# Optimization experiments

Measured on AMD Instinct MI355X. Metric: run time of the kernel, lower is better.

## Reference

```python
import jax, jax.numpy as jnp
import numpy as np

IN_FEATURES = 4096
OUT_FEATURES = 8192
LUT_SIZE = 65536  # 256 * 256 two-level codebook


def setup_inputs() -> dict:
    key = jax.random.key(0)
    k_x, k_b, k_f, k_s, k_l = jax.random.split(key, 5)
    x = jax.random.normal(k_x, (2, 256, IN_FEATURES), dtype=jnp.float32)
    base_idx = jax.random.randint(k_b, (OUT_FEATURES, IN_FEATURES), 0, 256, dtype=jnp.int32)
    fine_idx = jax.random.randint(k_f, (OUT_FEATURES, IN_FEATURES), 0, 256, dtype=jnp.int32)
    scale = jax.random.uniform(k_s, (OUT_FEATURES, 1), dtype=jnp.float32)
    lut = jax.random.normal(k_l, (LUT_SIZE,), dtype=jnp.float32)
    return {"x": x, "base_idx": base_idx, "fine_idx": fine_idx, "scale": scale, "lut": lut}


def reference(x, base_idx, fine_idx, scale, lut):
    # Two-level LUT dequant: combined 16-bit index = base*256 + fine
    combined_idx = base_idx * 256 + fine_idx              # [out, in] int32
    weights = lut[combined_idx] * scale                   # [out, in] fp32, per-row scale
    # F.linear(x, weights) == x @ weights.T
    return jnp.einsum('bsi,oi->bso', x, weights)
```

## Files before the change

kernel.cpp:

```cpp
#include <hip/hip_runtime.h>

typedef unsigned short ushort_t;
typedef unsigned int   uint32;
typedef __attribute__((ext_vector_type(8)))  short short8;
typedef __attribute__((ext_vector_type(4)))  float floatx4;
typedef __attribute__((ext_vector_type(16))) float floatx16;

#define IN_F   4096
#define OUT_F  8192
#define M_TOT  512

__device__ __forceinline__ ushort_t f2bf(float f) {
    uint32 u = __builtin_bit_cast(uint32, f);
    u += 0x7FFFu + ((u >> 16) & 1u);
    return (ushort_t)(u >> 16);
}
__device__ __forceinline__ uint32 pack2bf(float a, float b) {
    return (uint32)f2bf(a) | ((uint32)f2bf(b) << 16);
}

__global__ void cvt_x_kernel(const float* __restrict__ x, ushort_t* __restrict__ xb) {
    int i = (blockIdx.x * 256 + threadIdx.x) * 8;
    float4 v0 = *(const float4*)(x + i);
    float4 v1 = *(const float4*)(x + i + 4);
    short8 s;
    s[0] = (short)f2bf(v0.x); s[1] = (short)f2bf(v0.y);
    s[2] = (short)f2bf(v0.z); s[3] = (short)f2bf(v0.w);
    s[4] = (short)f2bf(v1.x); s[5] = (short)f2bf(v1.y);
    s[6] = (short)f2bf(v1.z); s[7] = (short)f2bf(v1.w);
    *(short8*)(xb + i) = s;
}

__global__ __launch_bounds__(1024, 4)
void dequant_kernel(const int* __restrict__ base_idx, const int* __restrict__ fine_idx,
                    const float* __restrict__ lut, ushort_t* __restrict__ wq)
{
    __shared__ ushort_t sh_lut[65536];
    const int tid = threadIdx.x;
#pragma unroll
    for (int i = tid * 4; i < 65536; i += 1024 * 4) {
        float4 v = *(const float4*)(lut + i);
        *(uint32*)&sh_lut[i]     = pack2bf(v.x, v.y);
        *(uint32*)&sh_lut[i + 2] = pack2bf(v.z, v.w);
    }

    const int row = blockIdx.x * 32 + (tid >> 5);
    const int c0  = (tid & 31) * 8;
    const int* bp = base_idx + (size_t)row * IN_F + c0;
    const int* fp = fine_idx + (size_t)row * IN_F + c0;
    ushort_t*  op = wq       + (size_t)row * IN_F + c0;

    int4 cb[4][2], cf[4][2];
#pragma unroll
    for (int d = 0; d < 4; ++d) {
        cb[d][0] = *(const int4*)(bp + d * 256);
        cb[d][1] = *(const int4*)(bp + d * 256 + 4);
        cf[d][0] = *(const int4*)(fp + d * 256);
        cf[d][1] = *(const int4*)(fp + d * 256 + 4);
    }
    __syncthreads();

#pragma unroll
    for (int u = 0; u < 16; ++u) {
        const int s = u & 3;
        const int4 b0 = cb[s][0], b1 = cb[s][1];
        const int4 f0 = cf[s][0], f1 = cf[s][1];
        if (u + 4 < 16) {
            cb[s][0] = *(const int4*)(bp + (u + 4) * 256);
            cb[s][1] = *(const int4*)(bp + (u + 4) * 256 + 4);
            cf[s][0] = *(const int4*)(fp + (u + 4) * 256);
            cf[s][1] = *(const int4*)(fp + (u + 4) * 256 + 4);
        }
        uint32 w0 = (uint32)sh_lut[(b0.x << 8) + f0.x]
                  | ((uint32)sh_lut[(b0.y << 8) + f0.y] << 16);
        uint32 w1 = (uint32)sh_lut[(b0.z << 8) + f0.z]
                  | ((uint32)sh_lut[(b0.w << 8) + f0.w] << 16);
        uint32 w2 = (uint32)sh_lut[(b1.x << 8) + f1.x]
                  | ((uint32)sh_lut[(b1.y << 8) + f1.y] << 16);
        uint32 w3 = (uint32)sh_lut[(b1.z << 8) + f1.z]
                  | ((uint32)sh_lut[(b1.w << 8) + f1.w] << 16);
        uint4 wv; wv.x = w0; wv.y = w1; wv.z = w2; wv.w = w3;
        *(uint4*)(op + u * 256) = wv;
    }
}

#define BK 128
__global__ __launch_bounds__(256, 2)
void gemm_split_kernel(const ushort_t* __restrict__ xb, const ushort_t* __restrict__ wq,
                       float* __restrict__ part)
{
    __shared__ ushort_t shA[128 * BK];
    __shared__ ushort_t shB[128 * BK];

    const int tid  = threadIdx.x;
    const int wave = tid >> 6;
    const int m0   = blockIdx.x * 128;
    const int n0   = blockIdx.y * 128;
    const int kz   = blockIdx.z * (IN_F / 2);

    const int g = (tid & 15) ^ ((tid >> 4) & 7);
    const ushort_t* aBase = xb + (size_t)(m0 + (tid >> 4)) * IN_F + kz + g * 8;
    const ushort_t* bBase = wq + (size_t)(n0 + (tid >> 4)) * IN_F + kz + g * 8;
    typedef __attribute__((address_space(3))) ushort_t lds_us;
    typedef const __attribute__((address_space(1))) void gvoid;
    lds_us* sA3 = (lds_us*)shA;
    lds_us* sB3 = (lds_us*)shB;

    const int lane = tid & 63;
    const int l31  = lane & 31;
    const int lhi  = lane >> 5;
    const int qm   = wave & 1;
    const int qn   = wave >> 1;
    const int rx   = l31 & 7;

    floatx16 acc[2][2];
    const floatx16 z16 = {0.f,0.f,0.f,0.f,0.f,0.f,0.f,0.f,0.f,0.f,0.f,0.f,0.f,0.f,0.f,0.f};
    acc[0][0] = z16; acc[0][1] = z16; acc[1][0] = z16; acc[1][1] = z16;

    for (int kb = 0; kb < IN_F / 2; kb += BK) {
#pragma unroll
        for (int i = 0; i < 8; ++i) {
            __builtin_amdgcn_global_load_lds((gvoid*)(aBase + (size_t)i * 16 * IN_F + kb),
                (__attribute__((address_space(3))) void*)(sA3 + i * 2048 + wave * 512),
                16, 0, 0);
            __builtin_amdgcn_global_load_lds((gvoid*)(bBase + (size_t)i * 16 * IN_F + kb),
                (__attribute__((address_space(3))) void*)(sB3 + i * 2048 + wave * 512),
                16, 0, 0);
        }
        __syncthreads();

#pragma unroll
        for (int ks = 0; ks < 8; ++ks) {
            const int p = ((2 * ks + lhi) ^ rx) * 8;
            short8 a0 = *(const short8*)&shA[(qm * 64 +      l31) * BK + p];
            short8 a1 = *(const short8*)&shA[(qm * 64 + 32 + l31) * BK + p];
            short8 b0 = *(const short8*)&shB[(qn * 64 +      l31) * BK + p];
            short8 b1 = *(const short8*)&shB[(qn * 64 + 32 + l31) * BK + p];
            acc[0][0] = __builtin_amdgcn_mfma_f32_32x32x16_bf16(a0, b0, acc[0][0], 0, 0, 0);
            acc[0][1] = __builtin_amdgcn_mfma_f32_32x32x16_bf16(a0, b1, acc[0][1], 0, 0, 0);
            acc[1][0] = __builtin_amdgcn_mfma_f32_32x32x16_bf16(a1, b0, acc[1][0], 0, 0, 0);
            acc[1][1] = __builtin_amdgcn_mfma_f32_32x32x16_bf16(a1, b1, acc[1][1], 0, 0, 0);
        }
        __syncthreads();
    }

    float* pz = part + (size_t)blockIdx.z * M_TOT * OUT_F;
#pragma unroll
    for (int nt = 0; nt < 2; ++nt) {
        const int col = n0 + qn * 64 + nt * 32 + l31;
#pragma unroll
        for (int mt = 0; mt < 2; ++mt) {
            const int rbase = m0 + qm * 64 + mt * 32 + 4 * lhi;
#pragma unroll
            for (int reg = 0; reg < 16; ++reg) {
                const int row = rbase + (reg & 3) + 8 * (reg >> 2);
                pz[(size_t)row * OUT_F + col] = acc[mt][nt][reg];
            }
        }
    }
}

__global__ void reduce_kernel(const float* __restrict__ p0, const float* __restrict__ p1,
                              const float* __restrict__ scale, float* __restrict__ out)
{
    const int i = (blockIdx.x * 256 + threadIdx.x) * 4;
    float4 a = *(const float4*)(p0 + i);
    float4 b = *(const float4*)(p1 + i);
    float4 s = *(const float4*)(scale + (i & (OUT_F - 1)));
    float4 r;
    r.x = (a.x + b.x) * s.x;
    r.y = (a.y + b.y) * s.y;
    r.z = (a.z + b.z) * s.z;
    r.w = (a.w + b.w) * s.w;
    *(float4*)(out + i) = r;
}

__global__ __launch_bounds__(256)
void gemm_full_kernel(const ushort_t* __restrict__ xb, const ushort_t* __restrict__ wq,
                      const float* __restrict__ scale, float* __restrict__ out)
{
    __shared__ ushort_t shA[128 * BK];
    __shared__ ushort_t shB[128 * BK];

    const int tid  = threadIdx.x;
    const int wave = tid >> 6;
    const int m0   = blockIdx.x * 128;
    const int n0   = blockIdx.y * 128;

    const int g = (tid & 15) ^ ((tid >> 4) & 7);
    const ushort_t* aBase = xb + (size_t)(m0 + (tid >> 4)) * IN_F + g * 8;
    const ushort_t* bBase = wq + (size_t)(n0 + (tid >> 4)) * IN_F + g * 8;
    typedef __attribute__((address_space(3))) ushort_t lds_us;
    typedef const __attribute__((address_space(1))) void gvoid;
    lds_us* sA3 = (lds_us*)shA;
    lds_us* sB3 = (lds_us*)shB;

    const int lane = tid & 63;
    const int l31  = lane & 31;
    const int lhi  = lane >> 5;
    const int qm   = wave & 1;
    const int qn   = wave >> 1;
    const int rx   = l31 & 7;

    floatx16 acc[2][2];
    const floatx16 z16 = {0.f,0.f,0.f,0.f,0.f,0.f,0.f,0.f,0.f,0.f,0.f,0.f,0.f,0.f,0.f,0.f};
    acc[0][0] = z16; acc[0][1] = z16; acc[1][0] = z16; acc[1][1] = z16;

    for (int kb = 0; kb < IN_F; kb += BK) {
#pragma unroll
        for (int i = 0; i < 8; ++i) {
            __builtin_amdgcn_global_load_lds((gvoid*)(aBase + (size_t)i * 16 * IN_F + kb),
                (__attribute__((address_space(3))) void*)(sA3 + i * 2048 + wave * 512), 16, 0, 0);
            __builtin_amdgcn_global_load_lds((gvoid*)(bBase + (size_t)i * 16 * IN_F + kb),
                (__attribute__((address_space(3))) void*)(sB3 + i * 2048 + wave * 512), 16, 0, 0);
        }
        __syncthreads();
#pragma unroll
        for (int ks = 0; ks < 8; ++ks) {
            const int p = ((2 * ks + lhi) ^ rx) * 8;
            short8 a0 = *(const short8*)&shA[(qm * 64 +      l31) * BK + p];
            short8 a1 = *(const short8*)&shA[(qm * 64 + 32 + l31) * BK + p];
            short8 b0 = *(const short8*)&shB[(qn * 64 +      l31) * BK + p];
            short8 b1 = *(const short8*)&shB[(qn * 64 + 32 + l31) * BK + p];
            acc[0][0] = __builtin_amdgcn_mfma_f32_32x32x16_bf16(a0, b0, acc[0][0], 0, 0, 0);
            acc[0][1] = __builtin_amdgcn_mfma_f32_32x32x16_bf16(a0, b1, acc[0][1], 0, 0, 0);
            acc[1][0] = __builtin_amdgcn_mfma_f32_32x32x16_bf16(a1, b0, acc[1][0], 0, 0, 0);
            acc[1][1] = __builtin_amdgcn_mfma_f32_32x32x16_bf16(a1, b1, acc[1][1], 0, 0, 0);
        }
        __syncthreads();
    }
#pragma unroll
    for (int nt = 0; nt < 2; ++nt) {
        const int col = n0 + qn * 64 + nt * 32 + l31;
        const float sc = scale[col];
#pragma unroll
        for (int mt = 0; mt < 2; ++mt) {
            const int rbase = m0 + qm * 64 + mt * 32 + 4 * lhi;
#pragma unroll
            for (int reg = 0; reg < 16; ++reg) {
                const int row = rbase + (reg & 3) + 8 * (reg >> 2);
                out[(size_t)row * OUT_F + col] = acc[mt][nt][reg] * sc;
            }
        }
    }
}

#define NB  32
#define FBK 128
#define WS  136
#define NITER (IN_F / FBK)
template<bool XBF16>
__global__ __launch_bounds__(1024, 4)
void ghost_kernel(const float* __restrict__ xf, const ushort_t* __restrict__ xb,
                  const int* __restrict__ base_idx, const int* __restrict__ fine_idx,
                  const float* __restrict__ scale, const float* __restrict__ lut,
                  float* __restrict__ out)
{
    __shared__ ushort_t sh_lut[65536];
    __shared__ ushort_t sh_w[2][NB * WS];
    const int tid = threadIdx.x;
    const int n0  = blockIdx.x * NB;
    for (int i = tid * 4; i < 65536; i += 1024 * 4) {
        float4 v = *(const float4*)(lut + i);
        sh_lut[i + 0] = f2bf(v.x); sh_lut[i + 1] = f2bf(v.y);
        sh_lut[i + 2] = f2bf(v.z); sh_lut[i + 3] = f2bf(v.w);
    }
    const int sn  = tid >> 5;
    const int skq = (tid & 31) * 4;
    const int* bp = base_idx + (size_t)(n0 + sn) * IN_F + skq;
    const int* fp = fine_idx + (size_t)(n0 + sn) * IN_F + skq;
    __syncthreads();
    int4 pb = *(const int4*)(bp);
    int4 pf = *(const int4*)(fp);
    {
        uint32 w0 = (uint32)sh_lut[(pb.x << 8) + pf.x] | ((uint32)sh_lut[(pb.y << 8) + pf.y] << 16);
        uint32 w1 = (uint32)sh_lut[(pb.z << 8) + pf.z] | ((uint32)sh_lut[(pb.w << 8) + pf.w] << 16);
        uint2 wv; wv.x = w0; wv.y = w1;
        *(uint2*)&sh_w[0][sn * WS + skq] = wv;
    }
    pb = *(const int4*)(bp + FBK);
    pf = *(const int4*)(fp + FBK);
    __syncthreads();
    const int lane = tid & 63;
    const int wave = tid >> 6;
    const int l16  = lane & 15;
    const int quad = lane >> 4;
    floatx4 acc[2][2];
    const floatx4 zero = {0.f, 0.f, 0.f, 0.f};
    acc[0][0] = zero; acc[0][1] = zero; acc[1][0] = zero; acc[1][1] = zero;
    const int mrow = wave * 32 + l16;
    const ushort_t* xrow  = XBF16 ? (xb + (size_t)mrow * IN_F + quad * 8) : (const ushort_t*)nullptr;
    const float*    xrowf = XBF16 ? (const float*)nullptr : (xf + (size_t)mrow * IN_F + quad * 8);
    for (int t = 0; t < NITER; ++t) {
        const int k0 = t * FBK;
        {
            uint32 w0 = (uint32)sh_lut[(pb.x << 8) + pf.x] | ((uint32)sh_lut[(pb.y << 8) + pf.y] << 16);
            uint32 w1 = (uint32)sh_lut[(pb.z << 8) + pf.z] | ((uint32)sh_lut[(pb.w << 8) + pf.w] << 16);
            uint2 wv; wv.x = w0; wv.y = w1;
            *(uint2*)&sh_w[(t + 1) & 1][sn * WS + skq] = wv;
        }
        {
            const int kk = (t + 2 < NITER ? t + 2 : NITER - 1) * FBK;
            pb = *(const int4*)(bp + kk);
            pf = *(const int4*)(fp + kk);
        }
        const ushort_t* wb = sh_w[t & 1];
#pragma unroll
        for (int ks = 0; ks < 4; ++ks) {
            const int kk = k0 + ks * 32;
            short8 b0 = *(const short8*)&wb[l16        * WS + ks * 32 + quad * 8];
            short8 b1 = *(const short8*)&wb[(16 + l16) * WS + ks * 32 + quad * 8];
            short8 a0, a1;
            if (XBF16) {
                a0 = *(const short8*)(xrow + kk);
                a1 = *(const short8*)(xrow + (size_t)16 * IN_F + kk);
            } else {
                const float* p0 = xrowf + kk;
                const float* p1 = xrowf + (size_t)16 * IN_F + kk;
                float4 u0 = *(const float4*)p0, u1 = *(const float4*)(p0 + 4);
                float4 v0 = *(const float4*)p1, v1 = *(const float4*)(p1 + 4);
                a0[0] = (short)f2bf(u0.x); a0[1] = (short)f2bf(u0.y);
                a0[2] = (short)f2bf(u0.z); a0[3] = (short)f2bf(u0.w);
                a0[4] = (short)f2bf(u1.x); a0[5] = (short)f2bf(u1.y);
                a0[6] = (short)f2bf(u1.z); a0[7] = (short)f2bf(u1.w);
                a1[0] = (short)f2bf(v0.x); a1[1] = (short)f2bf(v0.y);
                a1[2] = (short)f2bf(v0.z); a1[3] = (short)f2bf(v0.w);
                a1[4] = (short)f2bf(v1.x); a1[5] = (short)f2bf(v1.y);
                a1[6] = (short)f2bf(v1.z); a1[7] = (short)f2bf(v1.w);
            }
            acc[0][0] = __builtin_amdgcn_mfma_f32_16x16x32_bf16(a0, b0, acc[0][0], 0, 0, 0);
            acc[0][1] = __builtin_amdgcn_mfma_f32_16x16x32_bf16(a0, b1, acc[0][1], 0, 0, 0);
            acc[1][0] = __builtin_amdgcn_mfma_f32_16x16x32_bf16(a1, b0, acc[1][0], 0, 0, 0);
            acc[1][1] = __builtin_amdgcn_mfma_f32_16x16x32_bf16(a1, b1, acc[1][1], 0, 0, 0);
        }
        __syncthreads();
    }
#pragma unroll
    for (int nf = 0; nf < 2; ++nf) {
        const int col = n0 + nf * 16 + l16;
        const float sc = scale[col];
#pragma unroll
        for (int f = 0; f < 2; ++f) {
            const int r0 = wave * 32 + f * 16 + quad * 4;
#pragma unroll
            for (int r = 0; r < 4; ++r) {
                out[(size_t)(r0 + r) * OUT_F + col] = acc[f][nf][r] * sc;
            }
        }
    }
}

extern "C" void kernel_launch(void* const* d_in, const int* in_sizes, int n_in,
                              void* d_out, int out_size, void* d_ws, size_t ws_size,
                              hipStream_t stream) {
    const float* x      = (const float*)d_in[0];
    const int*   bidx   = (const int*)d_in[1];
    const int*   fidx   = (const int*)d_in[2];
    const float* scale  = (const float*)d_in[3];
    const float* lut    = (const float*)d_in[4];
    float*       out    = (float*)d_out;

    const size_t xb_bytes = (size_t)M_TOT * IN_F * sizeof(ushort_t);
    const size_t wq_bytes = (size_t)OUT_F * IN_F * sizeof(ushort_t);
    const size_t pt_bytes = (size_t)M_TOT * OUT_F * sizeof(float);

    if (ws_size >= xb_bytes + wq_bytes + 2 * pt_bytes) {
        ushort_t* xbuf = (ushort_t*)d_ws;
        ushort_t* wbuf = (ushort_t*)((char*)d_ws + xb_bytes);
        float*    part = (float*)((char*)d_ws + xb_bytes + wq_bytes);
        cvt_x_kernel<<<1024, 256, 0, stream>>>(x, xbuf);
        dequant_kernel<<<256, 1024, 0, stream>>>(bidx, fidx, lut, wbuf);
        gemm_split_kernel<<<dim3(4, 64, 2), 256, 0, stream>>>(xbuf, wbuf, part);
        reduce_kernel<<<(M_TOT * OUT_F) / (256 * 4), 256, 0, stream>>>(
            part, part + (size_t)M_TOT * OUT_F, scale, out);
    } else if (ws_size >= xb_bytes + wq_bytes) {
        ushort_t* xbuf = (ushort_t*)d_ws;
        ushort_t* wbuf = (ushort_t*)((char*)d_ws + xb_bytes);
        cvt_x_kernel<<<1024, 256, 0, stream>>>(x, xbuf);
        dequant_kernel<<<256, 1024, 0, stream>>>(bidx, fidx, lut, wbuf);
        gemm_full_kernel<<<dim3(4, 64), 256, 0, stream>>>(xbuf, wbuf, scale, out);
    } else if (ws_size >= xb_bytes) {
        ushort_t* xbuf = (ushort_t*)d_ws;
        cvt_x_kernel<<<1024, 256, 0, stream>>>(x, xbuf);
        ghost_kernel<true><<<OUT_F / NB, 1024, 0, stream>>>(x, xbuf, bidx, fidx, scale, lut, out);
    } else {
        ghost_kernel<false><<<OUT_F / NB, 1024, 0, stream>>>(x, nullptr, bidx, fidx, scale, lut, out);
    }
}
```

Before: 364.3 us.

## Fuse LUT dequantization into GEMM and tile x layout for direct loads

Replaces the separate dequant, split-K GEMM and reduction kernels with a single fused kernel that dequantizes weight tiles into shared memory via the bf16 LUT and immediately feeds MFMA, double-buffering the weight tile. x is converted to bf16 in a tiled layout so A fragments are read straight from global memory. This removes writing and re-reading the dequantized weight matrix and split-K partials, at the cost of low occupancy (one 1024-thread block per CU due to the LUT), a barrier per small k step, and repeated global reads of x across blocks.

New measurement: 344.6 us. 1.06x faster.

```diff
diff --git a/kernel.cpp b/kernel.cpp
--- a/kernel.cpp
+++ b/kernel.cpp
@@ -20,228 +20,107 @@
 }
 
 __global__ void cvt_x_kernel(const float* __restrict__ x, ushort_t* __restrict__ xb) {
-    int i = (blockIdx.x * 256 + threadIdx.x) * 8;
-    float4 v0 = *(const float4*)(x + i);
-    float4 v1 = *(const float4*)(x + i + 4);
+    const int g  = blockIdx.x * 256 + threadIdx.x;
+    const int r  = g >> 9;
+    const int k0 = (g & 511) * 8;
+    float4 v0 = *(const float4*)(x + (size_t)r * IN_F + k0);
+    float4 v1 = *(const float4*)(x + (size_t)r * IN_F + k0 + 4);
     short8 s;
     s[0] = (short)f2bf(v0.x); s[1] = (short)f2bf(v0.y);
     s[2] = (short)f2bf(v0.z); s[3] = (short)f2bf(v0.w);
     s[4] = (short)f2bf(v1.x); s[5] = (short)f2bf(v1.y);
     s[6] = (short)f2bf(v1.z); s[7] = (short)f2bf(v1.w);
-    *(short8*)(xb + i) = s;
+    const int mt = r >> 5;
+    const int kt = k0 >> 4;
+    ushort_t* dst = xb + ((size_t)(mt * 256 + kt) * 32 + (r & 31)) * 16 + (k0 & 15);
+    *(short8*)dst = s;
 }
 
 __global__ __launch_bounds__(1024, 4)
-void dequant_kernel(const int* __restrict__ base_idx, const int* __restrict__ fine_idx,
-                    const float* __restrict__ lut, ushort_t* __restrict__ wq)
+void fused_kernel(const ushort_t* __restrict__ xb, const int* __restrict__ base_idx,
+                  const int* __restrict__ fine_idx, const float* __restrict__ lut,
+                  const float* __restrict__ scale, float* __restrict__ out)
 {
     __shared__ ushort_t sh_lut[65536];
-    const int tid = threadIdx.x;
-#pragma unroll
-    for (int i = tid * 4; i < 65536; i += 1024 * 4) {
+    __shared__ ushort_t sh_w[2][32 * 64];
+
+    const int tid  = threadIdx.x;
+    const int nblk = blockIdx.x;
+
+    for (int i = tid * 4; i < 65536; i += 4096) {
         float4 v = *(const float4*)(lut + i);
         *(uint32*)&sh_lut[i]     = pack2bf(v.x, v.y);
         *(uint32*)&sh_lut[i + 2] = pack2bf(v.z, v.w);
     }
 
-    const int row = blockIdx.x * 32 + (tid >> 5);
-    const int c0  = (tid & 31) * 8;
-    const int* bp = base_idx + (size_t)row * IN_F + c0;
-    const int* fp = fine_idx + (size_t)row * IN_F + c0;
-    ushort_t*  op = wq       + (size_t)row * IN_F + c0;
-
-    int4 cb[4][2], cf[4][2];
-#pragma unroll
-    for (int d = 0; d < 4; ++d) {
-        cb[d][0] = *(const int4*)(bp + d * 256);
-        cb[d][1] = *(const int4*)(bp + d * 256 + 4);
-        cf[d][0] = *(const int4*)(fp + d * 256);
-        cf[d][1] = *(const int4*)(fp + d * 256 + 4);
-    }
-    __syncthreads();
-
-#pragma unroll
-    for (int u = 0; u < 16; ++u) {
-        const int s = u & 3;
-        const int4 b0 = cb[s][0], b1 = cb[s][1];
-        const int4 f0 = cf[s][0], f1 = cf[s][1];
-        if (u + 4 < 16) {
-            cb[s][0] = *(const int4*)(bp + (u + 4) * 256);
-            cb[s][1] = *(const int4*)(bp + (u + 4) * 256 + 4);
-            cf[s][0] = *(const int4*)(fp + (u + 4) * 256);
-            cf[s][1] = *(const int4*)(fp + (u + 4) * 256 + 4);
-        }
-        uint32 w0 = (uint32)sh_lut[(b0.x << 8) + f0.x]
-                  | ((uint32)sh_lut[(b0.y << 8) + f0.y] << 16);
-        uint32 w1 = (uint32)sh_lut[(b0.z << 8) + f0.z]
-                  | ((uint32)sh_lut[(b0.w << 8) + f0.w] << 16);
-        uint32 w2 = (uint32)sh_lut[(b1.x << 8) + f1.x]
-                  | ((uint32)sh_lut[(b1.y << 8) + f1.y] << 16);
-        uint32 w3 = (uint32)sh_lut[(b1.z << 8) + f1.z]
-                  | ((uint32)sh_lut[(b1.w << 8) + f1.w] << 16);
-        uint4 wv; wv.x = w0; wv.y = w1; wv.z = w2; wv.w = w3;
-        *(uint4*)(op + u * 256) = wv;
-    }
-}
-
-#define BK 128
-__global__ __launch_bounds__(256, 2)
-void gemm_split_kernel(const ushort_t* __restrict__ xb, const ushort_t* __restrict__ wq,
-                       float* __restrict__ part)
-{
-    __shared__ ushort_t shA[128 * BK];
-    __shared__ ushort_t shB[128 * BK];
-
-    const int tid  = threadIdx.x;
+    const int colr = tid >> 5;
+    const int kp   = (tid & 31) * 2;
+    const int2* bp = (const int2*)(base_idx + (size_t)(nblk * 32 + colr) * IN_F + kp);
+    const int2* fp = (const int2*)(fine_idx + (size_t)(nblk * 32 + colr) * IN_F + kp);
+    int2 cb = bp[0],  cf = fp[0];
+    int2 nb = bp[32], nf = fp[32];
+
+    const int woff = colr * 64 + ((((kp >> 3) ^ (colr & 7))) << 3) + (kp & 7);
+
+    const int lane = tid & 63;
     const int wave = tid >> 6;
-    const int m0   = blockIdx.x * 128;
-    const int n0   = blockIdx.y * 128;
-    const int kz   = blockIdx.z * (IN_F / 2);
-
-    const int g = (tid & 15) ^ ((tid >> 4) & 7);
-    const ushort_t* aBase = xb + (size_t)(m0 + (tid >> 4)) * IN_F + kz + g * 8;
-    const ushort_t* bBase = wq + (size_t)(n0 + (tid >> 4)) * IN_F + kz + g * 8;
-    typedef __attribute__((address_space(3))) ushort_t lds_us;
-    typedef const __attribute__((address_space(1))) void gvoid;
-    lds_us* sA3 = (lds_us*)shA;
-    lds_us* sB3 = (lds_us*)shB;
-
-    const int lane = tid & 63;
     const int l31  = lane & 31;
     const int lhi  = lane >> 5;
-    const int qm   = wave & 1;
-    const int qn   = wave >> 1;
-    const int rx   = l31 & 7;
-
-    floatx16 acc[2][2];
-    const floatx16 z16 = {0.f,0.f,0.f,0.f,0.f,0.f,0.f,0.f,0.f,0.f,0.f,0.f,0.f,0.f,0.f,0.f};
-    acc[0][0] = z16; acc[0][1] = z16; acc[1][0] = z16; acc[1][1] = z16;
-
-    for (int kb = 0; kb < IN_F / 2; kb += BK) {
-#pragma unroll
-        for (int i = 0; i < 8; ++i) {
-            __builtin_amdgcn_global_load_lds((gvoid*)(aBase + (size_t)i * 16 * IN_F + kb),
-                (__attribute__((address_space(3))) void*)(sA3 + i * 2048 + wave * 512),
-                16, 0, 0);
-            __builtin_amdgcn_global_load_lds((gvoid*)(bBase + (size_t)i * 16 * IN_F + kb),
-                (__attribute__((address_space(3))) void*)(sB3 + i * 2048 + wave * 512),
-                16, 0, 0);
-        }
+
+    __syncthreads();
+
+    {
+        uint32 w = (uint32)sh_lut[(cb.x << 8) + cf.x]
+                 | ((uint32)sh_lut[(cb.y << 8) + cf.y] << 16);
+        *(uint32*)&sh_w[0][woff] = w;
+    }
+    cb = nb; cf = nf;
+    nb = bp[64]; nf = fp[64];
+    __syncthreads();
+
+    floatx16 acc = {0.f,0.f,0.f,0.f,0.f,0.f,0.f,0.f,0.f,0.f,0.f,0.f,0.f,0.f,0.f,0.f};
+
+    const ushort_t* abase = xb + (size_t)wave * 256 * 512 + l31 * 16 + lhi * 8;
+    const int rx8 = (l31 & 7);
+
+#pragma unroll 2
+    for (int t = 0; t < 64; ++t) {
+        const int cur = t & 1;
+
+        short8 a0 = *(const short8*)(abase + (size_t)(t * 4 + 0) * 512);
+        short8 a1 = *(const short8*)(abase + (size_t)(t * 4 + 1) * 512);
+        short8 a2 = *(const short8*)(abase + (size_t)(t * 4 + 2) * 512);
+        short8 a3 = *(const short8*)(abase + (size_t)(t * 4 + 3) * 512);
+
+        const ushort_t* wb = sh_w[cur];
+        short8 b0 = *(const short8*)&wb[l31 * 64 + (((0 + lhi) ^ rx8) << 3)];
+        short8 b1 = *(const short8*)&wb[l31 * 64 + (((2 + lhi) ^ rx8) << 3)];
+        short8 b2 = *(const short8*)&wb[l31 * 64 + (((4 + lhi) ^ rx8) << 3)];
+        short8 b3 = *(const short8*)&wb[l31 * 64 + (((6 + lhi) ^ rx8) << 3)];
+
+        if (t + 1 < 64) {
+            uint32 w = (uint32)sh_lut[(cb.x << 8) + cf.x]
+                     | ((uint32)sh_lut[(cb.y << 8) + cf.y] << 16);
+            *(uint32*)&sh_w[cur ^ 1][woff] = w;
+            cb = nb; cf = nf;
+            if (t + 3 < 64) { nb = bp[(t + 3) * 32]; nf = fp[(t + 3) * 32]; }
+        }
+
+        acc = __builtin_amdgcn_mfma_f32_32x32x16_bf16(a0, b0, acc, 0, 0, 0);
+        acc = __builtin_amdgcn_mfma_f32_32x32x16_bf16(a1, b1, acc, 0, 0, 0);
+        acc = __builtin_amdgcn_mfma_f32_32x32x16_bf16(a2, b2, acc, 0, 0, 0);
+        acc = __builtin_amdgcn_mfma_f32_32x32x16_bf16(a3, b3, acc, 0, 0, 0);
+
         __syncthreads();
-
-#pragma unroll
-        for (int ks = 0; ks < 8; ++ks) {
-            const int p = ((2 * ks + lhi) ^ rx) * 8;
-            short8 a0 = *(const short8*)&shA[(qm * 64 +      l31) * BK + p];
-            short8 a1 = *(const short8*)&shA[(qm * 64 + 32 + l31) * BK + p];
-            short8 b0 = *(const short8*)&shB[(qn * 64 +      l31) * BK + p];
-            short8 b1 = *(const short8*)&shB[(qn * 64 + 32 + l31) * BK + p];
-            acc[0][0] = __builtin_amdgcn_mfma_f32_32x32x16_bf16(a0, b0, acc[0][0], 0, 0, 0);
-            acc[0][1] = __builtin_amdgcn_mfma_f32_32x32x16_bf16(a0, b1, acc[0][1], 0, 0, 0);
-            acc[1][0] = __builtin_amdgcn_mfma_f32_32x32x16_bf16(a1, b0, acc[1][0], 0, 0, 0);
-            acc[1][1] = __builtin_amdgcn_mfma_f32_32x32x16_bf16(a1, b1, acc[1][1], 0, 0, 0);
-        }
-        __syncthreads();
-    }
-
-    float* pz = part + (size_t)blockIdx.z * M_TOT * OUT_F;
-#pragma unroll
-    for (int nt = 0; nt < 2; ++nt) {
-        const int col = n0 + qn * 64 + nt * 32 + l31;
-#pragma unroll
-        for (int mt = 0; mt < 2; ++mt) {
-            const int rbase = m0 + qm * 64 + mt * 32 + 4 * lhi;
-#pragma unroll
-            for (int reg = 0; reg < 16; ++reg) {
-                const int row = rbase + (reg & 3) + 8 * (reg >> 2);
-                pz[(size_t)row * OUT_F + col] = acc[mt][nt][reg];
-            }
-        }
-    }
-}
-
-__global__ void reduce_kernel(const float* __restrict__ p0, const float* __restrict__ p1,
-                              const float* __restrict__ scale, float* __restrict__ out)
-{
-    const int i = (blockIdx.x * 256 + threadIdx.x) * 4;
-    float4 a = *(const float4*)(p0 + i);
-    float4 b = *(const float4*)(p1 + i);
-    float4 s = *(const float4*)(scale + (i & (OUT_F - 1)));
-    float4 r;
-    r.x = (a.x + b.x) * s.x;
-    r.y = (a.y + b.y) * s.y;
-    r.z = (a.z + b.z) * s.z;
-    r.w = (a.w + b.w) * s.w;
-    *(float4*)(out + i) = r;
-}
-
-__global__ __launch_bounds__(256)
-void gemm_full_kernel(const ushort_t* __restrict__ xb, const ushort_t* __restrict__ wq,
-                      const float* __restrict__ scale, float* __restrict__ out)
-{
-    __shared__ ushort_t shA[128 * BK];
-    __shared__ ushort_t shB[128 * BK];
-
-    const int tid  = threadIdx.x;
-    const int wave = tid >> 6;
-    const int m0   = blockIdx.x * 128;
-    const int n0   = blockIdx.y * 128;
-
-    const int g = (tid & 15) ^ ((tid >> 4) & 7);
-    const ushort_t* aBase = xb + (size_t)(m0 + (tid >> 4)) * IN_F + g * 8;
-    const ushort_t* bBase = wq + (size_t)(n0 + (tid >> 4)) * IN_F + g * 8;
-    typedef __attribute__((address_space(3))) ushort_t lds_us;
-    typedef const __attribute__((address_space(1))) void gvoid;
-    lds_us* sA3 = (lds_us*)shA;
-    lds_us* sB3 = (lds_us*)shB;
-
-    const int lane = tid & 63;
-    const int l31  = lane & 31;
-    const int lhi  = lane >> 5;
-    const int qm   = wave & 1;
-    const int qn   = wave >> 1;
-    const int rx   = l31 & 7;
-
-    floatx16 acc[2][2];
-    const floatx16 z16 = {0.f,0.f,0.f,0.f,0.f,0.f,0.f,0.f,0.f,0.f,0.f,0.f,0.f,0.f,0.f,0.f};
-    acc[0][0] = z16; acc[0][1] = z16; acc[1][0] = z16; acc[1][1] = z16;
-
-    for (int kb = 0; kb < IN_F; kb += BK) {
-#pragma unroll
-        for (int i = 0; i < 8; ++i) {
-            __builtin_amdgcn_global_load_lds((gvoid*)(aBase + (size_t)i * 16 * IN_F + kb),
-                (__attribute__((address_space(3))) void*)(sA3 + i * 2048 + wave * 512), 16, 0, 0);
-            __builtin_amdgcn_global_load_lds((gvoid*)(bBase + (size_t)i * 16 * IN_F + kb),
-                (__attribute__((address_space(3))) void*)(sB3 + i * 2048 + wave * 512), 16, 0, 0);
-        }
-        __syncthreads();
-#pragma unroll
-        for (int ks = 0; ks < 8; ++ks) {
-            const int p = ((2 * ks + lhi) ^ rx) * 8;
-            short8 a0 = *(const short8*)&shA[(qm * 64 +      l31) * BK + p];
-            short8 a1 = *(const short8*)&shA[(qm * 64 + 32 + l31) * BK + p];
-            short8 b0 = *(const short8*)&shB[(qn * 64 +      l31) * BK + p];
-            short8 b1 = *(const short8*)&shB[(qn * 64 + 32 + l31) * BK + p];
-            acc[0][0] = __builtin_amdgcn_mfma_f32_32x32x16_bf16(a0, b0, acc[0][0], 0, 0, 0);
-            acc[0][1] = __builtin_amdgcn_mfma_f32_32x32x16_bf16(a0, b1, acc[0][1], 0, 0, 0);
-            acc[1][0] = __builtin_amdgcn_mfma_f32_32x32x16_bf16(a1, b0, acc[1][0], 0, 0, 0);
-            acc[1][1] = __builtin_amdgcn_mfma_f32_32x32x16_bf16(a1, b1, acc[1][1], 0, 0, 0);
-        }
-        __syncthreads();
-    }
-#pragma unroll
-    for (int nt = 0; nt < 2; ++nt) {
-        const int col = n0 + qn * 64 + nt * 32 + l31;
-        const float sc = scale[col];
-#pragma unroll
-        for (int mt = 0; mt < 2; ++mt) {
-            const int rbase = m0 + qm * 64 + mt * 32 + 4 * lhi;
-#pragma unroll
-            for (int reg = 0; reg < 16; ++reg) {
-                const int row = rbase + (reg & 3) + 8 * (reg >> 2);
-                out[(size_t)row * OUT_F + col] = acc[mt][nt][reg] * sc;
-            }
-        }
+    }
+
+    const float sc = scale[nblk * 32 + l31];
+    float* op = out + (size_t)(nblk * 32 + l31);
+    const int rbase = wave * 32 + 4 * lhi;
+#pragma unroll
+    for (int reg = 0; reg < 16; ++reg) {
+        const int row = rbase + (reg & 3) + 8 * (reg >> 2);
+        op[(size_t)row * OUT_F] = acc[reg] * sc;
     }
 }
 
@@ -249,9 +128,8 @@
 #define FBK 128
 #define WS  136
 #define NITER (IN_F / FBK)
-template<bool XBF16>
 __global__ __launch_bounds__(1024, 4)
-void ghost_kernel(const float* __restrict__ xf, const ushort_t* __restrict__ xb,
+void ghost_kernel(const float* __restrict__ xf,
                   const int* __restrict__ base_idx, const int* __restrict__ fine_idx,
                   const float* __restrict__ scale, const float* __restrict__ lut,
                   float* __restrict__ out)
@@ -289,8 +167,7 @@
     const floatx4 zero = {0.f, 0.f, 0.f, 0.f};
     acc[0][0] = zero; acc[0][1] = zero; acc[1][0] = zero; acc[1][1] = zero;
     const int mrow = wave * 32 + l16;
-    const ushort_t* xrow  = XBF16 ? (xb + (size_t)mrow * IN_F + quad * 8) : (const ushort_t*)nullptr;
-    const float*    xrowf = XBF16 ? (const float*)nullptr : (xf + (size_t)mrow * IN_F + quad * 8);
+    const float* xrowf = xf + (size_t)mrow * IN_F + quad * 8;
     for (int t = 0; t < NITER; ++t) {
         const int k0 = t * FBK;
         {
@@ -311,23 +188,18 @@
             short8 b0 = *(const short8*)&wb[l16        * WS + ks * 32 + quad * 8];
             short8 b1 = *(const short8*)&wb[(16 + l16) * WS + ks * 32 + quad * 8];
             short8 a0, a1;
-            if (XBF16) {
-                a0 = *(const short8*)(xrow + kk);
-                a1 = *(const short8*)(xrow + (size_t)16 * IN_F + kk);
-            } else {
-                const float* p0 = xrowf + kk;
-                const float* p1 = xrowf + (size_t)16 * IN_F + kk;
-                float4 u0 = *(const float4*)p0, u1 = *(const float4*)(p0 + 4);
-                float4 v0 = *(const float4*)p1, v1 = *(const float4*)(p1 + 4);
-                a0[0] = (short)f2bf(u0.x); a0[1] = (short)f2bf(u0.y);
-                a0[2] = (short)f2bf(u0.z); a0[3] = (short)f2bf(u0.w);
-                a0[4] = (short)f2bf(u1.x); a0[5] = (short)f2bf(u1.y);
-                a0[6] = (short)f2bf(u1.z); a0[7] = (short)f2bf(u1.w);
-                a1[0] = (short)f2bf(v0.x); a1[1] = (short)f2bf(v0.y);
-                a1[2] = (short)f2bf(v0.z); a1[3] = (short)f2bf(v0.w);
-                a1[4] = (short)f2bf(v1.x); a1[5] = (short)f2bf(v1.y);
-                a1[6] = (short)f2bf(v1.z); a1[7] = (short)f2bf(v1.w);
-            }
+            const float* p0 = xrowf + kk;
+            const float* p1 = xrowf + (size_t)16 * IN_F + kk;
+            float4 u0 = *(const float4*)p0, u1 = *(const float4*)(p0 + 4);
+            float4 v0 = *(const float4*)p1, v1 = *(const float4*)(p1 + 4);
+            a0[0] = (short)f2bf(u0.x); a0[1] = (short)f2bf(u0.y);
+            a0[2] = (short)f2bf(u0.z); a0[3] = (short)f2bf(u0.w);
+            a0[4] = (short)f2bf(u1.x); a0[5] = (short)f2bf(u1.y);
+            a0[6] = (short)f2bf(u1.z); a0[7] = (short)f2bf(u1.w);
+            a1[0] = (short)f2bf(v0.x); a1[1] = (short)f2bf(v0.y);
+            a1[2] = (short)f2bf(v0.z); a1[3] = (short)f2bf(v0.w);
+            a1[4] = (short)f2bf(v1.x); a1[5] = (short)f2bf(v1.y);
+            a1[6] = (short)f2bf(v1.z); a1[7] = (short)f2bf(v1.w);
             acc[0][0] = __builtin_amdgcn_mfma_f32_16x16x32_bf16(a0, b0, acc[0][0], 0, 0, 0);
             acc[0][1] = __builtin_amdgcn_mfma_f32_16x16x32_bf16(a0, b1, acc[0][1], 0, 0, 0);
             acc[1][0] = __builtin_amdgcn_mfma_f32_16x16x32_bf16(a1, b0, acc[1][0], 0, 0, 0);
@@ -361,29 +233,12 @@
     float*       out    = (float*)d_out;
 
     const size_t xb_bytes = (size_t)M_TOT * IN_F * sizeof(ushort_t);
-    const size_t wq_bytes = (size_t)OUT_F * IN_F * sizeof(ushort_t);
-    const size_t pt_bytes = (size_t)M_TOT * OUT_F * sizeof(float);
-
-    if (ws_size >= xb_bytes + wq_bytes + 2 * pt_bytes) {
-        ushort_t* xbuf = (ushort_t*)d_ws;
-        ushort_t* wbuf = (ushort_t*)((char*)d_ws + xb_bytes);
-        float*    part = (float*)((char*)d_ws + xb_bytes + wq_bytes);
-        cvt_x_kernel<<<1024, 256, 0, stream>>>(x, xbuf);
-        dequant_kernel<<<256, 1024, 0, stream>>>(bidx, fidx, lut, wbuf);
-        gemm_split_kernel<<<dim3(4, 64, 2), 256, 0, stream>>>(xbuf, wbuf, part);
-        reduce_kernel<<<(M_TOT * OUT_F) / (256 * 4), 256, 0, stream>>>(
-            part, part + (size_t)M_TOT * OUT_F, scale, out);
-    } else if (ws_size >= xb_bytes + wq_bytes) {
-        ushort_t* xbuf = (ushort_t*)d_ws;
-        ushort_t* wbuf = (ushort_t*)((char*)d_ws + xb_bytes);
-        cvt_x_kernel<<<1024, 256, 0, stream>>>(x, xbuf);
-        dequant_kernel<<<256, 1024, 0, stream>>>(bidx, fidx, lut, wbuf);
-        gemm_full_kernel<<<dim3(4, 64), 256, 0, stream>>>(xbuf, wbuf, scale, out);
-    } else if (ws_size >= xb_bytes) {
+
+    if (ws_size >= xb_bytes) {
         ushort_t* xbuf = (ushort_t*)d_ws;
         cvt_x_kernel<<<1024, 256, 0, stream>>>(x, xbuf);
-        ghost_kernel<true><<<OUT_F / NB, 1024, 0, stream>>>(x, xbuf, bidx, fidx, scale, lut, out);
+        fused_kernel<<<256, 1024, 0, stream>>>(xbuf, bidx, fidx, lut, scale, out);
     } else {
-        ghost_kernel<false><<<OUT_F / NB, 1024, 0, stream>>>(x, nullptr, bidx, fidx, scale, lut, out);
-    }
-}
+        ghost_kernel<<<OUT_F / NB, 1024, 0, stream>>>(x, bidx, fidx, scale, lut, out);
+    }
+}
```
